# Kernel tuning notes

Measured on AMD Instinct MI355X. Metric: run time of the kernel, lower is better.

Reference implementation:

```python
import jax, jax.numpy as jnp
import numpy as np
from jax import lax

BN_EPS = 1e-5
K_TOP = 2


def _conv_bn_relu_pool(x, w, b, g, beta, mean, var):
    # x: [B,C,H,W], w: [O,I,3,3]; SAME conv -> eval BN -> ReLU -> 2x2 maxpool
    y = lax.conv_general_dilated(x, w, (1, 1), 'SAME',
                                 dimension_numbers=('NCHW', 'OIHW', 'NCHW'))
    y = y + b[None, :, None, None]
    inv = g / jnp.sqrt(var + BN_EPS)
    y = (y - mean[None, :, None, None]) * inv[None, :, None, None] + beta[None, :, None, None]
    y = jax.nn.relu(y)
    return lax.reduce_window(y, -jnp.inf, lax.max, (1, 1, 2, 2), (1, 1, 2, 2), 'VALID')


def setup_inputs() -> dict:
    key = jax.random.key(0)
    ks = jax.random.split(key, 12)
    B, F_DIM, H_DIM, OUT, E = 4096, 128, 64, 10, 8
    d = {}
    d['x'] = jax.random.normal(ks[0], (B, 3, 32, 32), dtype=jnp.float32)
    # conv stacks
    def conv_block(k, cin, cout, i):
        kk = jax.random.split(k, 2)
        d[f'conv{i}_w'] = jax.random.normal(kk[0], (cout, cin, 3, 3), dtype=jnp.float32) * (1.0 / np.sqrt(cin * 9))
        d[f'conv{i}_b'] = jnp.zeros((cout,), dtype=jnp.float32)
        d[f'bn{i}_g'] = jnp.ones((cout,), dtype=jnp.float32)
        d[f'bn{i}_b'] = jnp.zeros((cout,), dtype=jnp.float32)
        d[f'bn{i}_m'] = jax.random.normal(kk[1], (cout,), dtype=jnp.float32) * 0.1
        d[f'bn{i}_v'] = jnp.ones((cout,), dtype=jnp.float32)
    conv_block(ks[1], 3, 32, 1)
    conv_block(ks[2], 32, 64, 2)
    conv_block(ks[3], 64, 128, 3)
    # experts (stacked): MLPHead Linear(128,64) -> ReLU -> Linear(64,10)
    d['w1'] = jax.random.normal(ks[4], (E, F_DIM, H_DIM), dtype=jnp.float32) * (1.0 / np.sqrt(F_DIM))
    d['b1'] = jnp.zeros((E, H_DIM), dtype=jnp.float32)
    d['w2'] = jax.random.normal(ks[5], (E, H_DIM, OUT), dtype=jnp.float32) * (1.0 / np.sqrt(H_DIM))
    d['b2'] = jnp.zeros((E, OUT), dtype=jnp.float32)
    # top-k gate: Linear(128, 8)
    d['gate_w'] = jax.random.normal(ks[6], (F_DIM, E), dtype=jnp.float32) * (1.0 / np.sqrt(F_DIM))
    d['gate_b'] = jnp.zeros((E,), dtype=jnp.float32)
    return d


def reference(x, conv1_w, conv1_b, bn1_g, bn1_b, bn1_m, bn1_v,
              conv2_w, conv2_b, bn2_g, bn2_b, bn2_m, bn2_v,
              conv3_w, conv3_b, bn3_g, bn3_b, bn3_m, bn3_v,
              w1, b1, w2, b2, gate_w, gate_b):
    # Backbone: 3x32x32 -> 128 (eval-mode BN, dropout identity)
    h = _conv_bn_relu_pool(x, conv1_w, conv1_b, bn1_g, bn1_b, bn1_m, bn1_v)  # [B,32,16,16]
    h = _conv_bn_relu_pool(h, conv2_w, conv2_b, bn2_g, bn2_b, bn2_m, bn2_v)  # [B,64,8,8]
    h = _conv_bn_relu_pool(h, conv3_w, conv3_b, bn3_g, bn3_b, bn3_m, bn3_v)  # [B,128,4,4]
    feat = jnp.mean(h, axis=(2, 3))  # AdaptiveAvgPool2d(1) + Flatten -> [B,128]

    # Top-k gate: logits -> top-k -> softmax over selected -> scatter to [B,E]
    logits = feat @ gate_w + gate_b                     # [B,E]
    vals, idx = lax.top_k(logits, K_TOP)                # [B,k]
    wk = jax.nn.softmax(vals, axis=-1)                  # [B,k]
    B, E = logits.shape
    weights = jnp.zeros((B, E), dtype=logits.dtype)
    weights = weights.at[jnp.arange(B)[:, None], idx].set(wk)

    # Dense expert MLPs (as in source), gate-weighted sum
    he = jax.nn.relu(jnp.einsum('bf,efh->beh', feat, w1) + b1[None])  # [B,E,H]
    oe = jnp.einsum('beh,eho->beo', he, w2) + b2[None]                # [B,E,O]
    return jnp.einsum('be,beo->bo', weights, oe)                      # [B,O]
```

## Files before the change

### kernel.cpp

```cpp
#include <hip/hip_runtime.h>
#include <math.h>

typedef __attribute__((ext_vector_type(8))) short short8;
typedef __attribute__((ext_vector_type(4))) float f32x4;
#define MFMA __builtin_amdgcn_mfma_f32_16x16x32_bf16

#define BN_EPS 1e-5f

static const size_t W1C2_OFF = 0;
static const size_t W2C2_OFF = 1024;
static const size_t W3C2_OFF = 19456;
static const size_t B1_OFF   = 93184;
static const size_t B2_OFF   = 93216;
static const size_t B3_OFF   = 93280;

__device__ inline unsigned short rneb(float x) {
    unsigned u = __float_as_uint(x);
    return (unsigned short)((u + 0x7FFFu + ((u >> 16) & 1u)) >> 16);
}
__device__ inline float b2f(unsigned short h) {
    return __uint_as_float(((unsigned)h) << 16);
}

__global__ __launch_bounds__(256) void k_prep(
    const float* __restrict__ c1w, const float* __restrict__ c2w, const float* __restrict__ c3w,
    const float* __restrict__ c1b, const float* __restrict__ g1, const float* __restrict__ be1,
    const float* __restrict__ m1, const float* __restrict__ v1,
    const float* __restrict__ c2b, const float* __restrict__ g2, const float* __restrict__ be2,
    const float* __restrict__ m2, const float* __restrict__ v2,
    const float* __restrict__ c3b, const float* __restrict__ g3, const float* __restrict__ be3,
    const float* __restrict__ m3, const float* __restrict__ v3,
    unsigned short* __restrict__ w1c2, unsigned short* __restrict__ w2c2,
    unsigned short* __restrict__ w3c2,
    float* __restrict__ b1c, float* __restrict__ b2c, float* __restrict__ b3c)
{
    int i = blockIdx.x * 256 + threadIdx.x;
    if (i < 2048) {
        int e = i & 7, p = (i >> 3) & 1, kc = (i >> 4) & 3, ol = (i >> 6) & 15, n = i >> 10;
        int o = n * 16 + ol, k = kc * 8 + e;
        float s = g1[o] * rsqrtf(v1[o] + BN_EPS);
        float wv = (k < 27) ? c1w[o * 27 + k] * s : 0.f;
        unsigned short h = rneb(wv);
        w1c2[i] = p ? rneb(wv - b2f(h)) : h;
        return;
    }
    i -= 2048;
    if (i < 36864) {
        int e = i & 7, p = (i >> 3) & 1, kc = (i >> 4) & 3, ol = (i >> 6) & 15;
        int n = (i >> 10) & 3, tap = i >> 12;
        int o = n * 16 + ol, ci = kc * 8 + e;
        float s = g2[o] * rsqrtf(v2[o] + BN_EPS);
        float wv = c2w[o * 288 + ci * 9 + tap] * s;
        unsigned short h = rneb(wv);
        w2c2[i] = p ? rneb(wv - b2f(h)) : h;
        return;
    }
    i -= 36864;
    if (i < 147456) {
        int e = i & 7, p = (i >> 3) & 1, kc = (i >> 4) & 3, ol = (i >> 6) & 15;
        int nf = (i >> 10) & 7, s_ = (i >> 13) & 1, tap = i >> 14;
        int o = nf * 16 + ol, ci = s_ * 32 + kc * 8 + e;
        float sc = g3[o] * rsqrtf(v3[o] + BN_EPS);
        float wv = c3w[o * 576 + ci * 9 + tap] * sc;
        unsigned short h = rneb(wv);
        w3c2[i] = p ? rneb(wv - b2f(h)) : h;
        return;
    }
    i -= 147456;
    if (i < 32) { float s = g1[i]*rsqrtf(v1[i]+BN_EPS); b1c[i] = (c1b[i]-m1[i])*s + be1[i]; return; }
    i -= 32;
    if (i < 64) { float s = g2[i]*rsqrtf(v2[i]+BN_EPS); b2c[i] = (c2b[i]-m2[i])*s + be2[i]; return; }
    i -= 64;
    if (i < 128) { float s = g3[i]*rsqrtf(v3[i]+BN_EPS); b3c[i] = (c3b[i]-m3[i])*s + be3[i]; return; }
}

__global__ __launch_bounds__(512, 6) void k_fused(
    const float* __restrict__ x,
    const unsigned short* __restrict__ w1c2,
    const unsigned short* __restrict__ w2c2,
    const unsigned short* __restrict__ w3c2,
    const float* __restrict__ b1c, const float* __restrict__ b2c, const float* __restrict__ b3c,
    const float* __restrict__ w1e, const float* __restrict__ b1e,
    const float* __restrict__ w2e, const float* __restrict__ b2e,
    const float* __restrict__ gw, const float* __restrict__ gb,
    float* __restrict__ out)
{
    __shared__ __align__(16) unsigned short R1[20736];
    __shared__ __align__(16) unsigned int   R2x[3074];
    float* sFeat = (float*)R2x;
    float* sOutB = (float*)R2x + 128;
    float* sPart = (float*)R2x + 160;

    const int b = blockIdx.x, t = threadIdx.x;
    const int lane = t & 63, w = t >> 6;
    const int l15 = lane & 15, lg = lane >> 4;
    const int4 z4 = {0, 0, 0, 0};

    {
        const float* xb = x + (size_t)b * 3072;
        for (int i = t; i < 3072; i += 512) {
            float v = xb[i];
            unsigned short h = rneb(v);
            unsigned short lo = rneb(v - b2f(h));
            R2x[i] = ((unsigned)h << 16) | lo;
        }
        if (t == 0) R2x[3072] = 0;
        for (int hh = t; hh < 272; hh += 512) {
            int pr = hh >> 2, kc = hh & 3;
            int py, px;
            if (pr < 36) { py = (pr < 18) ? 0 : 17; px = (pr < 18) ? pr : pr - 18; }
            else { int r = pr - 36; py = 1 + (r >> 1); px = (r & 1) ? 17 : 0; }
            int ei = ((py * 4 + kc) * 18 + px) * 8;
            *(int4*)(R1 + ei) = z4;
            *(int4*)(R1 + 10368 + ei) = z4;
        }
    }
    __syncthreads();

    {
        short8 b1h[2], b1l[2];
#pragma unroll
        for (int n = 0; n < 2; n++) {
            const short8* bp = (const short8*)(w1c2 + 16 * ((n * 16 + l15) * 4 + lg));
            b1h[n] = bp[0]; b1l[n] = bp[1];
        }
        int dyE[8], dxE[8], cbE[8];
#pragma unroll
        for (int e = 0; e < 8; e++) {
            int k = lg * 8 + e;
            if (k < 27) { int ci = k / 9, tp = k - ci * 9;
                          dyE[e] = tp / 3 - 1; dxE[e] = tp % 3 - 1; cbE[e] = ci << 10; }
            else { dyE[e] = -1000; dxE[e] = 0; cbE[e] = 0; }
        }
        float bia[2] = { b1c[l15], b1c[16 + l15] };
#pragma unroll 1
        for (int q = 0; q < 2; q++) {
            int m0 = 8 * w + 4 * q;
            f32x4 acc[4][2];
#pragma unroll
            for (int mi = 0; mi < 4; mi++)
#pragma unroll
                for (int n = 0; n < 2; n++) acc[mi][n] = (f32x4)0.f;
#pragma unroll
            for (int mi = 0; mi < 4; mi++) {
                int pos = 16 * (m0 + mi) + l15, py = pos >> 5, px = pos & 31;
                short8 ah, al;
#pragma unroll
                for (int e = 0; e < 8; e++) {
                    int yy = py + dyE[e], xv = px + dxE[e];
                    int idx = cbE[e] + (yy << 5) + xv;
                    bool ok = ((unsigned)yy < 32u) && ((unsigned)xv < 32u);
                    unsigned u = R2x[ok ? idx : 3072];
                    ah[e] = (short)(u >> 16);
                    al[e] = (short)(u & 0xFFFFu);
                }
#pragma unroll
                for (int n = 0; n < 2; n++) {
                    acc[mi][n] = MFMA(ah, b1h[n], acc[mi][n], 0, 0, 0);
                    acc[mi][n] = MFMA(ah, b1l[n], acc[mi][n], 0, 0, 0);
                    acc[mi][n] = MFMA(al, b1h[n], acc[mi][n], 0, 0, 0);
                }
            }
            int PY = 2 * w + q;
#pragma unroll
            for (int n = 0; n < 2; n++) {
                int o = n * 16 + l15;
#pragma unroll
                for (int h = 0; h < 2; h++)
#pragma unroll
                for (int jp = 0; jp < 2; jp++) {
                    float v00 = fmaxf(acc[h][n][2*jp]     + bia[n], 0.f);
                    float v01 = fmaxf(acc[h][n][2*jp + 1] + bia[n], 0.f);
                    float v10 = fmaxf(acc[h+2][n][2*jp]     + bia[n], 0.f);
                    float v11 = fmaxf(acc[h+2][n][2*jp + 1] + bia[n], 0.f);
                    float pm = fmaxf(fmaxf(v00, v01), fmaxf(v10, v11));
                    int PX = h * 8 + lg * 2 + jp;
                    unsigned short ph = rneb(pm), pl = rneb(pm - b2f(ph));
                    int ei = (((PY + 1) * 4 + (o >> 3)) * 18 + (PX + 1)) * 8 + (o & 7);
                    R1[ei] = ph; R1[10368 + ei] = pl;
                }
            }
        }
    }
    __syncthreads();

    {
        const int mh = w & 1, nn = w >> 1;
        f32x4 acc2[8];
#pragma unroll
        for (int mi = 0; mi < 8; mi++) acc2[mi] = (f32x4)0.f;
        const unsigned short* wb = w2c2 + ((size_t)(nn * 16 + l15) * 4 + lg) * 16;
        const int abase = (mh * 8) * 576 + lg * 144 + l15 * 8;
        short8 bhA, blA, bhB, blB;
#define LDB2(tp, BH, BL) { const short8* bp = (const short8*)(wb + (tp) * 4096); BH = bp[0]; BL = bp[1]; }
#define CMP2(tp, BH, BL) { int dy_ = (tp) / 3, dx_ = (tp) - 3 * dy_; \
        int roff_ = dy_ * 576 + dx_ * 8; \
        _Pragma("unroll") for (int mi = 0; mi < 8; mi++) { \
            int ea_ = abase + mi * 576 + roff_; \
            short8 ah_ = *(const short8*)(R1 + ea_); \
            short8 al_ = *(const short8*)(R1 + 10368 + ea_); \
            acc2[mi] = MFMA(ah_, BH, acc2[mi], 0, 0, 0); \
            acc2[mi] = MFMA(ah_, BL, acc2[mi], 0, 0, 0); \
            acc2[mi] = MFMA(al_, BH, acc2[mi], 0, 0, 0); } }
        LDB2(0, bhA, blA);
#pragma unroll 1
        for (int tp = 0; tp < 8; tp += 2) {
            LDB2(tp + 1, bhB, blB);
            CMP2(tp, bhA, blA);
            LDB2(tp + 2, bhA, blA);
            CMP2(tp + 1, bhB, blB);
        }
        CMP2(8, bhA, blA);
        __syncthreads();
        for (int hh = t; hh < 288; hh += 512) {
            int pr = hh >> 3, kc = hh & 7;
            int py, px;
            if (pr < 20) { py = (pr < 10) ? 0 : 9; px = (pr < 10) ? pr : pr - 10; }
            else { int r = pr - 20; py = 1 + (r >> 1); px = (r & 1) ? 9 : 0; }
            int ei = ((py * 8 + kc) * 11 + px) * 8;
            *(int4*)(R1 + ei) = z4;
            *(int4*)(R1 + 7040 + ei) = z4;
        }
        {
            int o = nn * 16 + l15;
            float bia = b2c[o];
#pragma unroll
            for (int mi2 = 0; mi2 < 4; mi2++) {
                int PY = mh * 4 + mi2;
#pragma unroll
                for (int jp = 0; jp < 2; jp++) {
                    float v00 = fmaxf(acc2[2*mi2][2*jp]     + bia, 0.f);
                    float v01 = fmaxf(acc2[2*mi2][2*jp + 1] + bia, 0.f);
                    float v10 = fmaxf(acc2[2*mi2+1][2*jp]     + bia, 0.f);
                    float v11 = fmaxf(acc2[2*mi2+1][2*jp + 1] + bia, 0.f);
                    float pm = fmaxf(fmaxf(v00, v01), fmaxf(v10, v11));
                    int PX = lg * 2 + jp;
                    unsigned short ph = rneb(pm), pl = rneb(pm - b2f(ph));
                    int ei = (((PY + 1) * 8 + (o >> 3)) * 11 + (PX + 1)) * 8 + (o & 7);
                    R1[ei] = ph; R1[7040 + ei] = pl;
                }
            }
        }
    }
    __syncthreads();

    {
        const int nf = w;
        f32x4 acc3[4];
#pragma unroll
        for (int mi = 0; mi < 4; mi++) acc3[mi] = (f32x4)0.f;
        const unsigned short* wb3 = w3c2 + ((size_t)(nf * 16 + l15) * 4 + lg) * 16;
        const int py0 = (l15 >> 3), px3 = l15 & 7;
        short8 bhA, blA, bhB, blB;
#define LDB3(ii, BH, BL) { const short8* bp = (const short8*)(wb3 + (ii) * 8192); BH = bp[0]; BL = bp[1]; }
#define CMP3(ii, BH, BL) { int tap_ = (ii) >> 1, s_ = (ii) & 1; \
        int dy_ = tap_ / 3, dx_ = tap_ - 3 * dy_; \
        int roff_ = dy_ * 704 + (s_ * 4 + lg) * 88 + dx_ * 8 + px3 * 8; \
        _Pragma("unroll") for (int mi = 0; mi < 4; mi++) { \
            int ea_ = (mi * 2 + py0) * 704 + roff_; \
            short8 ah_ = *(const short8*)(R1 + ea_); \
            short8 al_ = *(const short8*)(R1 + 7040 + ea_); \
            acc3[mi] = MFMA(ah_, BH, acc3[mi], 0, 0, 0); \
            acc3[mi] = MFMA(ah_, BL, acc3[mi], 0, 0, 0); \
            acc3[mi] = MFMA(al_, BH, acc3[mi], 0, 0, 0); } }
        LDB3(0, bhA, blA);
#pragma unroll 1
        for (int ii = 0; ii < 16; ii += 2) {
            LDB3(ii + 1, bhB, blB);
            CMP3(ii, bhA, blA);
            LDB3(ii + 2, bhA, blA);
            CMP3(ii + 1, bhB, blB);
        }
        LDB3(17, bhB, blB);
        CMP3(16, bhA, blA);
        CMP3(17, bhB, blB);
        {
            int o = nf * 16 + l15;
            float bia = b3c[o];
            float featsum = 0.f;
#pragma unroll
            for (int mi = 0; mi < 4; mi++) {
                float sumv = 0.f;
#pragma unroll
                for (int jp = 0; jp < 2; jp++) {
                    float v0 = fmaxf(acc3[mi][2*jp]     + bia, 0.f);
                    float v1 = fmaxf(acc3[mi][2*jp + 1] + bia, 0.f);
                    float vm = fmaxf(v0, v1);
                    vm = fmaxf(vm, __shfl_xor(vm, 32, 64));
                    sumv += vm;
                }
                sumv += __shfl_xor(sumv, 16, 64);
                featsum += sumv;
            }
            if (lane < 16) sFeat[nf * 16 + lane] = featsum * (1.0f / 16.0f);
        }
    }
    __syncthreads();

    int i1 = 0, i2 = 0;
    float wk1 = 0.f, wk2 = 0.f;
    {
        float f0 = sFeat[lane], f1 = sFeat[64 + lane];
        float lgt[8];
#pragma unroll
        for (int e = 0; e < 8; e++) {
            float p = f0 * gw[lane * 8 + e] + f1 * gw[(64 + lane) * 8 + e];
#pragma unroll
            for (int s = 1; s < 64; s <<= 1) p += __shfl_xor(p, s, 64);
            lgt[e] = p + gb[e];
        }
        float v1m = -1e30f, v2m = -1e30f;
#pragma unroll
        for (int e = 0; e < 8; e++) {
            float le = lgt[e];
            if (le > v1m) { v2m = v1m; i2 = i1; v1m = le; i1 = e; }
            else if (le > v2m) { v2m = le; i2 = e; }
        }
        float ex = expf(v2m - v1m);
        wk1 = 1.f / (1.f + ex); wk2 = ex / (1.f + ex);
        int e = (w < 4) ? i1 : i2;
        int k0 = (w & 3) * 32;
        const float* W1 = w1e + (size_t)e * 8192 + (size_t)k0 * 64;
        float hj = 0.f;
#pragma unroll 8
        for (int kk = 0; kk < 32; kk++) hj += sFeat[k0 + kk] * W1[kk * 64 + lane];
        sPart[w * 64 + lane] = hj;
    }
    __syncthreads();
    if (w < 2) {
        int e = (w == 0) ? i1 : i2;
        float wk = (w == 0) ? wk1 : wk2;
        float hj = b1e[e * 64 + lane]
                 + sPart[(w * 4 + 0) * 64 + lane] + sPart[(w * 4 + 1) * 64 + lane]
                 + sPart[(w * 4 + 2) * 64 + lane] + sPart[(w * 4 + 3) * 64 + lane];
        hj = fmaxf(hj, 0.f);
        const float* W2 = w2e + (size_t)e * 640 + lane * 10;
#pragma unroll
        for (int o = 0; o < 10; o++) {
            float po = hj * W2[o];
#pragma unroll
            for (int s = 1; s < 64; s <<= 1) po += __shfl_xor(po, s, 64);
            if (lane == 0) sOutB[w * 10 + o] = wk * (po + b2e[e * 10 + o]);
        }
    }
    __syncthreads();
    if (t < 10) out[(size_t)b * 10 + t] = sOutB[t] + sOutB[10 + t];
}

extern "C" void kernel_launch(void* const* d_in, const int* in_sizes, int n_in,
                              void* d_out, int out_size, void* d_ws, size_t ws_size,
                              hipStream_t stream)
{
    const float* x   = (const float*)d_in[0];
    const float* c1w = (const float*)d_in[1];
    const float* c1b = (const float*)d_in[2];
    const float* g1  = (const float*)d_in[3];
    const float* be1 = (const float*)d_in[4];
    const float* m1  = (const float*)d_in[5];
    const float* v1  = (const float*)d_in[6];
    const float* c2w = (const float*)d_in[7];
    const float* c2b = (const float*)d_in[8];
    const float* g2  = (const float*)d_in[9];
    const float* be2 = (const float*)d_in[10];
    const float* m2  = (const float*)d_in[11];
    const float* v2  = (const float*)d_in[12];
    const float* c3w = (const float*)d_in[13];
    const float* c3b = (const float*)d_in[14];
    const float* g3  = (const float*)d_in[15];
    const float* be3 = (const float*)d_in[16];
    const float* m3  = (const float*)d_in[17];
    const float* v3  = (const float*)d_in[18];
    const float* w1e = (const float*)d_in[19];
    const float* b1e = (const float*)d_in[20];
    const float* w2e = (const float*)d_in[21];
    const float* b2e = (const float*)d_in[22];
    const float* gw  = (const float*)d_in[23];
    const float* gb  = (const float*)d_in[24];

    float* ws = (float*)d_ws;
    unsigned short* w1c2 = (unsigned short*)(ws + W1C2_OFF);
    unsigned short* w2c2 = (unsigned short*)(ws + W2C2_OFF);
    unsigned short* w3c2 = (unsigned short*)(ws + W3C2_OFF);
    float* b1c = ws + B1_OFF;
    float* b2c = ws + B2_OFF;
    float* b3c = ws + B3_OFF;

    k_prep<<<729, 256, 0, stream>>>(c1w, c2w, c3w,
                                    c1b, g1, be1, m1, v1,
                                    c2b, g2, be2, m2, v2,
                                    c3b, g3, be3, m3, v3,
                                    w1c2, w2c2, w3c2, b1c, b2c, b3c);
    k_fused<<<4096, 512, 0, stream>>>(x, w1c2, w2c2, w3c2, b1c, b2c, b3c,
                                      w1e, b1e, w2e, b2e, gw, gb, (float*)d_out);
}
```

Before: 318.6 us.

## Shrink shared memory via padded input and unpadded conv1 rows; split conv passes

The input image is stored in a zero-padded 34x34 layout so conv1 gathers need no bounds checks. The conv1 output buffer drops its padded top and bottom rows, and conv2 skips out-of-range taps with a branch instead, which shrinks total LDS. Conv1 and conv2 are split into two passes with smaller accumulator arrays to reduce register pressure. Conv2 pool results are held in registers until after a barrier, then written back. The aim is higher occupancy and fewer index computations, at the cost of more loop iterations and a divergent-looking tap guard in conv2.

```diff
diff --git a/kernel.cpp b/kernel.cpp
--- a/kernel.cpp
+++ b/kernel.cpp
@@ -20,6 +20,10 @@
 }
 __device__ inline float b2f(unsigned short h) {
     return __uint_as_float(((unsigned)h) << 16);
+}
+__device__ inline unsigned packhl(float v) {
+    unsigned short h = rneb(v);
+    return ((unsigned)h << 16) | (unsigned)rneb(v - b2f(h));
 }
 
 __global__ __launch_bounds__(256) void k_prep(
@@ -85,11 +89,11 @@
     const float* __restrict__ gw, const float* __restrict__ gb,
     float* __restrict__ out)
 {
-    __shared__ __align__(16) unsigned short R1[20736];
-    __shared__ __align__(16) unsigned int   R2x[3074];
-    float* sFeat = (float*)R2x;
-    float* sOutB = (float*)R2x + 128;
-    float* sPart = (float*)R2x + 160;
+    __shared__ __align__(16) unsigned short LDSU[25368];
+    unsigned* xs = (unsigned*)(LDSU + 18432);
+    float* sFeat = (float*)xs;
+    float* sPart = (float*)xs + 128;
+    float* sOutB = (float*)xs + 640;
 
     const int b = blockIdx.x, t = threadIdx.x;
     const int lane = t & 63, w = t >> 6;
@@ -99,20 +103,22 @@
     {
         const float* xb = x + (size_t)b * 3072;
         for (int i = t; i < 3072; i += 512) {
-            float v = xb[i];
-            unsigned short h = rneb(v);
-            unsigned short lo = rneb(v - b2f(h));
-            R2x[i] = ((unsigned)h << 16) | lo;
-        }
-        if (t == 0) R2x[3072] = 0;
-        for (int hh = t; hh < 272; hh += 512) {
-            int pr = hh >> 2, kc = hh & 3;
-            int py, px;
-            if (pr < 36) { py = (pr < 18) ? 0 : 17; px = (pr < 18) ? pr : pr - 18; }
-            else { int r = pr - 36; py = 1 + (r >> 1); px = (r & 1) ? 17 : 0; }
+            int ci = i >> 10, y = (i >> 5) & 31, xx = i & 31;
+            xs[ci * 1156 + (y + 1) * 34 + (xx + 1)] = packhl(xb[i]);
+        }
+        for (int hh = t; hh < 396; hh += 512) {
+            int ci = (hh * 31776) >> 22;
+            int r = hh - ci * 132;
+            int yy, xx;
+            if (r < 68) { yy = (r < 34) ? 0 : 33; xx = (r < 34) ? r : r - 34; }
+            else { int rr = r - 68; yy = 1 + (rr >> 1); xx = (rr & 1) ? 33 : 0; }
+            xs[ci * 1156 + yy * 34 + xx] = 0u;
+        }
+        for (int hh = t; hh < 128; hh += 512) {
+            int py = hh >> 3, kc = (hh >> 1) & 3, px = (hh & 1) ? 17 : 0;
             int ei = ((py * 4 + kc) * 18 + px) * 8;
-            *(int4*)(R1 + ei) = z4;
-            *(int4*)(R1 + 10368 + ei) = z4;
+            *(int4*)(LDSU + ei) = z4;
+            *(int4*)(LDSU + 9216 + ei) = z4;
         }
     }
     __syncthreads();
@@ -124,93 +130,104 @@
             const short8* bp = (const short8*)(w1c2 + 16 * ((n * 16 + l15) * 4 + lg));
             b1h[n] = bp[0]; b1l[n] = bp[1];
         }
-        int dyE[8], dxE[8], cbE[8];
+        int aoffU[8];
 #pragma unroll
         for (int e = 0; e < 8; e++) {
             int k = lg * 8 + e;
             if (k < 27) { int ci = k / 9, tp = k - ci * 9;
-                          dyE[e] = tp / 3 - 1; dxE[e] = tp % 3 - 1; cbE[e] = ci << 10; }
-            else { dyE[e] = -1000; dxE[e] = 0; cbE[e] = 0; }
+                          aoffU[e] = ci * 1156 + (tp / 3) * 34 + (tp % 3); }
+            else aoffU[e] = 0;
         }
         float bia[2] = { b1c[l15], b1c[16 + l15] };
 #pragma unroll 1
         for (int q = 0; q < 2; q++) {
-            int m0 = 8 * w + 4 * q;
-            f32x4 acc[4][2];
-#pragma unroll
-            for (int mi = 0; mi < 4; mi++)
-#pragma unroll
-                for (int n = 0; n < 2; n++) acc[mi][n] = (f32x4)0.f;
-#pragma unroll
-            for (int mi = 0; mi < 4; mi++) {
-                int pos = 16 * (m0 + mi) + l15, py = pos >> 5, px = pos & 31;
-                short8 ah, al;
-#pragma unroll
-                for (int e = 0; e < 8; e++) {
-                    int yy = py + dyE[e], xv = px + dxE[e];
-                    int idx = cbE[e] + (yy << 5) + xv;
-                    bool ok = ((unsigned)yy < 32u) && ((unsigned)xv < 32u);
-                    unsigned u = R2x[ok ? idx : 3072];
-                    ah[e] = (short)(u >> 16);
-                    al[e] = (short)(u & 0xFFFFu);
+#pragma unroll 1
+            for (int pp = 0; pp < 2; pp++) {
+                int m0 = 8 * w + 4 * q;
+                f32x4 acc[2][2];
+#pragma unroll
+                for (int ii = 0; ii < 2; ii++)
+#pragma unroll
+                    for (int n = 0; n < 2; n++) acc[ii][n] = (f32x4)0.f;
+#pragma unroll
+                for (int ii = 0; ii < 2; ii++) {
+                    int mi = pp + 2 * ii;
+                    int pos = 16 * (m0 + mi) + l15, py = pos >> 5, px = pos & 31;
+                    int base = py * 34 + px;
+                    short8 ah, al;
+#pragma unroll
+                    for (int e = 0; e < 8; e++) {
+                        unsigned u = xs[base + aoffU[e]];
+                        ah[e] = (short)(u >> 16);
+                        al[e] = (short)(u & 0xFFFFu);
+                    }
+#pragma unroll
+                    for (int n = 0; n < 2; n++) {
+                        acc[ii][n] = MFMA(ah, b1h[n], acc[ii][n], 0, 0, 0);
+                        acc[ii][n] = MFMA(ah, b1l[n], acc[ii][n], 0, 0, 0);
+                        acc[ii][n] = MFMA(al, b1h[n], acc[ii][n], 0, 0, 0);
+                    }
                 }
+                int PY = 2 * w + q;
 #pragma unroll
                 for (int n = 0; n < 2; n++) {
-                    acc[mi][n] = MFMA(ah, b1h[n], acc[mi][n], 0, 0, 0);
-                    acc[mi][n] = MFMA(ah, b1l[n], acc[mi][n], 0, 0, 0);
-                    acc[mi][n] = MFMA(al, b1h[n], acc[mi][n], 0, 0, 0);
+                    int o = n * 16 + l15;
+#pragma unroll
+                    for (int jp = 0; jp < 2; jp++) {
+                        float v00 = fmaxf(acc[0][n][2*jp]     + bia[n], 0.f);
+                        float v01 = fmaxf(acc[0][n][2*jp + 1] + bia[n], 0.f);
+                        float v10 = fmaxf(acc[1][n][2*jp]     + bia[n], 0.f);
+                        float v11 = fmaxf(acc[1][n][2*jp + 1] + bia[n], 0.f);
+                        float pm = fmaxf(fmaxf(v00, v01), fmaxf(v10, v11));
+                        int PX = pp * 8 + lg * 2 + jp;
+                        int ei = ((PY * 4 + (o >> 3)) * 18 + (PX + 1)) * 8 + (o & 7);
+                        unsigned short ph = rneb(pm);
+                        LDSU[ei] = ph;
+                        LDSU[9216 + ei] = rneb(pm - b2f(ph));
+                    }
                 }
             }
-            int PY = 2 * w + q;
-#pragma unroll
-            for (int n = 0; n < 2; n++) {
-                int o = n * 16 + l15;
-#pragma unroll
-                for (int h = 0; h < 2; h++)
-#pragma unroll
-                for (int jp = 0; jp < 2; jp++) {
-                    float v00 = fmaxf(acc[h][n][2*jp]     + bia[n], 0.f);
-                    float v01 = fmaxf(acc[h][n][2*jp + 1] + bia[n], 0.f);
-                    float v10 = fmaxf(acc[h+2][n][2*jp]     + bia[n], 0.f);
-                    float v11 = fmaxf(acc[h+2][n][2*jp + 1] + bia[n], 0.f);
-                    float pm = fmaxf(fmaxf(v00, v01), fmaxf(v10, v11));
-                    int PX = h * 8 + lg * 2 + jp;
-                    unsigned short ph = rneb(pm), pl = rneb(pm - b2f(ph));
-                    int ei = (((PY + 1) * 4 + (o >> 3)) * 18 + (PX + 1)) * 8 + (o & 7);
-                    R1[ei] = ph; R1[10368 + ei] = pl;
-                }
-            }
         }
     }
     __syncthreads();
 
     {
         const int mh = w & 1, nn = w >> 1;
-        f32x4 acc2[8];
-#pragma unroll
-        for (int mi = 0; mi < 8; mi++) acc2[mi] = (f32x4)0.f;
         const unsigned short* wb = w2c2 + ((size_t)(nn * 16 + l15) * 4 + lg) * 16;
-        const int abase = (mh * 8) * 576 + lg * 144 + l15 * 8;
+        float pmv0[4], pmv1[4];
         short8 bhA, blA, bhB, blB;
 #define LDB2(tp, BH, BL) { const short8* bp = (const short8*)(wb + (tp) * 4096); BH = bp[0]; BL = bp[1]; }
-#define CMP2(tp, BH, BL) { int dy_ = (tp) / 3, dx_ = (tp) - 3 * dy_; \
-        int roff_ = dy_ * 576 + dx_ * 8; \
-        _Pragma("unroll") for (int mi = 0; mi < 8; mi++) { \
-            int ea_ = abase + mi * 576 + roff_; \
-            short8 ah_ = *(const short8*)(R1 + ea_); \
-            short8 al_ = *(const short8*)(R1 + 10368 + ea_); \
-            acc2[mi] = MFMA(ah_, BH, acc2[mi], 0, 0, 0); \
-            acc2[mi] = MFMA(ah_, BL, acc2[mi], 0, 0, 0); \
-            acc2[mi] = MFMA(al_, BH, acc2[mi], 0, 0, 0); } }
-        LDB2(0, bhA, blA);
-#pragma unroll 1
-        for (int tp = 0; tp < 8; tp += 2) {
-            LDB2(tp + 1, bhB, blB);
-            CMP2(tp, bhA, blA);
-            LDB2(tp + 2, bhA, blA);
-            CMP2(tp + 1, bhB, blB);
-        }
-        CMP2(8, bhA, blA);
+#define CMP2(tp, BH, BL, ACC, MP) { int dy_ = (tp) / 3, dx_ = (tp) - 3 * dy_; \
+        _Pragma("unroll") for (int mii = 0; mii < 4; mii++) { \
+            int py1_ = mh * 8 + (MP) * 4 + mii + dy_ - 1; \
+            if ((unsigned)py1_ < 16u) { \
+                int ea_ = py1_ * 576 + lg * 144 + (l15 + dx_) * 8; \
+                short8 ah_ = *(const short8*)(LDSU + ea_); \
+                short8 al_ = *(const short8*)(LDSU + 9216 + ea_); \
+                ACC[mii] = MFMA(ah_, BH, ACC[mii], 0, 0, 0); \
+                ACC[mii] = MFMA(ah_, BL, ACC[mii], 0, 0, 0); \
+                ACC[mii] = MFMA(al_, BH, ACC[mii], 0, 0, 0); } } }
+#define P2PASS(MP, PMV) { \
+        f32x4 acc2[4]; \
+        _Pragma("unroll") for (int mi = 0; mi < 4; mi++) acc2[mi] = (f32x4)0.f; \
+        LDB2(0, bhA, blA); \
+        _Pragma("unroll 1") for (int tp = 0; tp < 8; tp += 2) { \
+            LDB2(tp + 1, bhB, blB); \
+            CMP2(tp, bhA, blA, acc2, MP); \
+            LDB2(tp + 2, bhA, blA); \
+            CMP2(tp + 1, bhB, blB, acc2, MP); \
+        } \
+        CMP2(8, bhA, blA, acc2, MP); \
+        { float bia_ = b2c[nn * 16 + l15]; \
+          _Pragma("unroll") for (int r = 0; r < 2; r++) \
+          _Pragma("unroll") for (int jp = 0; jp < 2; jp++) { \
+            float v00 = fmaxf(acc2[2*r][2*jp]     + bia_, 0.f); \
+            float v01 = fmaxf(acc2[2*r][2*jp + 1] + bia_, 0.f); \
+            float v10 = fmaxf(acc2[2*r+1][2*jp]     + bia_, 0.f); \
+            float v11 = fmaxf(acc2[2*r+1][2*jp + 1] + bia_, 0.f); \
+            PMV[r * 2 + jp] = fmaxf(fmaxf(v00, v01), fmaxf(v10, v11)); } } }
+        P2PASS(0, pmv0);
+        P2PASS(1, pmv1);
         __syncthreads();
         for (int hh = t; hh < 288; hh += 512) {
             int pr = hh >> 3, kc = hh & 7;
@@ -218,27 +235,24 @@
             if (pr < 20) { py = (pr < 10) ? 0 : 9; px = (pr < 10) ? pr : pr - 10; }
             else { int r = pr - 20; py = 1 + (r >> 1); px = (r & 1) ? 9 : 0; }
             int ei = ((py * 8 + kc) * 11 + px) * 8;
-            *(int4*)(R1 + ei) = z4;
-            *(int4*)(R1 + 7040 + ei) = z4;
+            *(int4*)(LDSU + ei) = z4;
+            *(int4*)(LDSU + 7040 + ei) = z4;
         }
         {
             int o = nn * 16 + l15;
-            float bia = b2c[o];
-#pragma unroll
-            for (int mi2 = 0; mi2 < 4; mi2++) {
-                int PY = mh * 4 + mi2;
-#pragma unroll
-                for (int jp = 0; jp < 2; jp++) {
-                    float v00 = fmaxf(acc2[2*mi2][2*jp]     + bia, 0.f);
-                    float v01 = fmaxf(acc2[2*mi2][2*jp + 1] + bia, 0.f);
-                    float v10 = fmaxf(acc2[2*mi2+1][2*jp]     + bia, 0.f);
-                    float v11 = fmaxf(acc2[2*mi2+1][2*jp + 1] + bia, 0.f);
-                    float pm = fmaxf(fmaxf(v00, v01), fmaxf(v10, v11));
-                    int PX = lg * 2 + jp;
-                    unsigned short ph = rneb(pm), pl = rneb(pm - b2f(ph));
-                    int ei = (((PY + 1) * 8 + (o >> 3)) * 11 + (PX + 1)) * 8 + (o & 7);
-                    R1[ei] = ph; R1[7040 + ei] = pl;
-                }
+#pragma unroll
+            for (int mp = 0; mp < 2; mp++)
+#pragma unroll
+            for (int r = 0; r < 2; r++)
+#pragma unroll
+            for (int jp = 0; jp < 2; jp++) {
+                float pm = (mp == 0) ? pmv0[r * 2 + jp] : pmv1[r * 2 + jp];
+                int PY = mh * 4 + mp * 2 + r;
+                int PX = lg * 2 + jp;
+                int ei = (((PY + 1) * 8 + (o >> 3)) * 11 + (PX + 1)) * 8 + (o & 7);
+                unsigned short ph = rneb(pm);
+                LDSU[ei] = ph;
+                LDSU[7040 + ei] = rneb(pm - b2f(ph));
             }
         }
     }
@@ -258,8 +272,8 @@
         int roff_ = dy_ * 704 + (s_ * 4 + lg) * 88 + dx_ * 8 + px3 * 8; \
         _Pragma("unroll") for (int mi = 0; mi < 4; mi++) { \
             int ea_ = (mi * 2 + py0) * 704 + roff_; \
-            short8 ah_ = *(const short8*)(R1 + ea_); \
-            short8 al_ = *(const short8*)(R1 + 7040 + ea_); \
+            short8 ah_ = *(const short8*)(LDSU + ea_); \
+            short8 al_ = *(const short8*)(LDSU + 7040 + ea_); \
             acc3[mi] = MFMA(ah_, BH, acc3[mi], 0, 0, 0); \
             acc3[mi] = MFMA(ah_, BL, acc3[mi], 0, 0, 0); \
             acc3[mi] = MFMA(al_, BH, acc3[mi], 0, 0, 0); } }
```

Result: no change. 324.7 us (+1.9%).
